# Optimization experiments

Measured on AMD Instinct MI355X. Metric: run time of the kernel, lower is better.

Reference implementation:

```python
import jax, jax.numpy as jnp
import numpy as np

B, C, H = 64, 64, 32

def _pm_cross_pairs(ks):
    # Replicates PM_cross(2, ks): pairs (i, i+j) ordered by gap j=1..ks-1, then i.
    a, b = [], []
    for j in range(1, ks):
        for i in range(ks - j):
            a.append(i)
            b.append(i + j)
    return np.array(a, dtype=np.int32), np.array(b, dtype=np.int32)

def setup_inputs() -> dict:
    key = jax.random.key(0)
    k1, k2 = jax.random.split(key)
    ia, ib = _pm_cross_pairs(H)           # 496 pairs for H=32
    hk = ia.shape[0] + 2 * H              # 560
    x = jax.random.normal(k1, (B, C, H, H), dtype=jnp.float32)
    weight = 0.1 * jax.random.normal(k2, (C, H, hk, H), dtype=jnp.float32)
    return {"x": x, "weight": weight, "idx_a": jnp.asarray(ia), "idx_b": jnp.asarray(ib)}

def reference(x, weight, idx_a, idx_b):
    # cross-term products along last axis: [B,C,H,P]
    cross = x[..., idx_a] * x[..., idx_b]
    feat = jnp.concatenate([x, x * x, cross], axis=-1)  # [B,C,H,Hk]
    # per-(channel,row) grouped matmul
    return jnp.einsum('bcij,cijo->bcio', feat, weight)
```

## Files before the change

kernel.cpp:

```cpp
#include <hip/hip_runtime.h>

#define NB 64
#define NC 64
#define NH 32
#define HK 560
#define NOCT 96
#define NCHUNK 12
#define XSTR 57

typedef __bf16 bf16x8 __attribute__((ext_vector_type(8)));
typedef float f32x4 __attribute__((ext_vector_type(4)));

__global__ __launch_bounds__(256, 5) void hconv_kernel(
    const float* __restrict__ x, const float* __restrict__ w,
    const int* __restrict__ idx_a, const int* __restrict__ idx_b,
    float* __restrict__ out)
{
    __shared__ float s_x[NB * XSTR];
    __shared__ unsigned s_desc[NOCT];
    __shared__ __align__(16) unsigned short s_wT[2][32][72];

    const int t = threadIdx.x;
    const int g = blockIdx.x;
    const int c = g >> 5, i = g & 31;

    {
        const int xrow = t >> 2, seg = t & 3;
        const float* xr = x + (((size_t)xrow * NC + c) * NH + i) * NH + seg * 8;
        float4 v0 = *(const float4*)(xr);
        float4 v1 = *(const float4*)(xr + 4);
        float* dst = &s_x[xrow * XSTR + 8 + seg * 8];
        dst[0] = v0.x; dst[1] = v0.y; dst[2] = v0.z; dst[3] = v0.w;
        dst[4] = v1.x; dst[5] = v1.y; dst[6] = v1.z; dst[7] = v1.w;
        if (seg == 0) {
            float* r0 = &s_x[xrow * XSTR];
            #pragma unroll
            for (int m = 0; m < 8; ++m) {
                r0[m] = 0.0f;
                r0[40 + m] = 0.0f;
                r0[48 + m] = 1.0f;
            }
        }
    }

    if (t < NOCT) {
        unsigned pa, pb, ko;
        if (t < 4)      { pa = 8u + 8u * t; pb = 48u; ko = 8u * t; }
        else if (t < 8) { unsigned u = t - 4; pa = pb = 8u + 8u * u; ko = 32u + 8u * u; }
        else if (t < 84) {
            unsigned q = t - 8, j, a;
            if (q < 28)      { j = 1 + q / 4;         a = q % 4; }
            else if (q < 52) { j = 8 + (q - 28) / 3;  a = (q - 28) % 3; }
            else if (q < 68) { j = 16 + (q - 52) / 2; a = (q - 52) % 2; }
            else             { j = 24 + (q - 68);     a = 0; }
            ko = 64u + (j - 1) * 32u - (j * (j - 1)) / 2u + 8u * a;
            pa = 8u + 8u * a; pb = pa + j;
            if (ko > 552u) { unsigned s = ko - 552u; ko = 552u; pa -= s; pb -= s; }
        } else { pa = 0u; pb = 0u; ko = 0u; }
        s_desc[t] = pa | (pb << 6) | (ko << 12);
    }

    const int wv = t >> 6, lane = t & 63;
    const int lr = lane & 15, lq = lane >> 4;
    const int arow = wv * 16 + lr;
    const int wo = t & 31;
    const int wkg = t >> 5;
    const float* wbase = w + (size_t)(c * NH + i) * HK * NH;
    const float* xrp = &s_x[arow * XSTR];

    __syncthreads();

    unsigned sd[NCHUNK];
    #pragma unroll
    for (int ch = 0; ch < NCHUNK; ++ch) sd[ch] = s_desc[ch * 8 + wkg] >> 12;

    float p0[8], p1[8];

    auto wload = [&](int ch, float* pv) {
        const float* p = wbase + (size_t)sd[ch] * NH + wo;
        #pragma unroll
        for (int r = 0; r < 8; ++r) pv[r] = p[r * NH];
    };
    auto wstore = [&](int bufi, const float* pv) {
        bf16x8 v;
        #pragma unroll
        for (int r = 0; r < 8; ++r) v[r] = (__bf16)pv[r];
        *(bf16x8*)&s_wT[bufi][wo][wkg * 8] = v;
    };

    f32x4 acc0 = {0.f, 0.f, 0.f, 0.f};
    f32x4 acc1 = {0.f, 0.f, 0.f, 0.f};

    auto mfma_chunk = [&](int ch, int bufi) {
        #pragma unroll
        for (int ks = 0; ks < 2; ++ks) {
            const unsigned d = s_desc[ch * 8 + ks * 4 + lq];
            const float* pA = xrp + (d & 63u);
            const float* pB = xrp + ((d >> 6) & 63u);
            bf16x8 a;
            #pragma unroll
            for (int j = 0; j < 8; ++j)
                a[j] = (__bf16)(pA[j] * pB[j]);
            bf16x8 b0 = *(const bf16x8*)&s_wT[bufi][lr][ks * 32 + lq * 8];
            bf16x8 b1 = *(const bf16x8*)&s_wT[bufi][16 + lr][ks * 32 + lq * 8];
            acc0 = __builtin_amdgcn_mfma_f32_16x16x32_bf16(a, b0, acc0, 0, 0, 0);
            acc1 = __builtin_amdgcn_mfma_f32_16x16x32_bf16(a, b1, acc1, 0, 0, 0);
        }
    };

    wload(0, p0);
    wload(1, p1);
    wstore(0, p0);
    __syncthreads();

    for (int it = 0; it < 6; ++it) {
        const int ca = 2 * it, cb = 2 * it + 1;
        wload(ca + 2 < NCHUNK ? ca + 2 : NCHUNK - 1, p0);
        mfma_chunk(ca, 0);
        wstore(1, p1);
        __syncthreads();
        wload(cb + 2 < NCHUNK ? cb + 2 : NCHUNK - 1, p1);
        mfma_chunk(cb, 1);
        wstore(0, p0);
        __syncthreads();
    }

    #pragma unroll
    for (int r = 0; r < 4; ++r) {
        const int b = wv * 16 + lq * 4 + r;
        float* op = out + (((size_t)b * NC + c) * NH + i) * NH;
        op[lr] = acc0[r];
        op[16 + lr] = acc1[r];
    }
}

extern "C" void kernel_launch(void* const* d_in, const int* in_sizes, int n_in,
                              void* d_out, int out_size, void* d_ws, size_t ws_size,
                              hipStream_t stream) {
    const float* x = (const float*)d_in[0];
    const float* w = (const float*)d_in[1];
    const int* idx_a = (const int*)d_in[2];
    const int* idx_b = (const int*)d_in[3];
    float* out = (float*)d_out;
    hconv_kernel<<<dim3(NC * NH), dim3(256), 0, stream>>>(x, w, idx_a, idx_b, out);
}
```

Baseline: 234.5 us.

## Split K across waves with register-direct weight loads and LDS reduction

Each wave now owns a slice of the K chunks and computes all 64 batch rows for all 32 outputs. Weights go from global memory straight into registers as MFMA B fragments, so the shared-memory transposed weight buffer and the per-chunk barriers are gone. A final LDS reduction across the four waves produces the output, which is written with float4 stores. The cost is more accumulator registers (launch bounds lowered to 4) and each wave computing the A-side products for every row, plus an extra reduction pass.

```diff
diff --git a/kernel.cpp b/kernel.cpp
--- a/kernel.cpp
+++ b/kernel.cpp
@@ -5,20 +5,19 @@
 #define NH 32
 #define HK 560
 #define NOCT 96
-#define NCHUNK 12
 #define XSTR 57
 
 typedef __bf16 bf16x8 __attribute__((ext_vector_type(8)));
 typedef float f32x4 __attribute__((ext_vector_type(4)));
 
-__global__ __launch_bounds__(256, 5) void hconv_kernel(
+__global__ __launch_bounds__(256, 4) void hconv_kernel(
     const float* __restrict__ x, const float* __restrict__ w,
     const int* __restrict__ idx_a, const int* __restrict__ idx_b,
     float* __restrict__ out)
 {
-    __shared__ float s_x[NB * XSTR];
-    __shared__ unsigned s_desc[NOCT];
-    __shared__ __align__(16) unsigned short s_wT[2][32][72];
+    __shared__ __align__(16) float smem[4 * 64 * 33];
+    float* s_x = smem;
+    unsigned* s_desc = (unsigned*)&smem[NB * XSTR];
 
     const int t = threadIdx.x;
     const int g = blockIdx.x;
@@ -45,92 +44,110 @@
 
     if (t < NOCT) {
         unsigned pa, pb, ko;
-        if (t < 4)      { pa = 8u + 8u * t; pb = 48u; ko = 8u * t; }
-        else if (t < 8) { unsigned u = t - 4; pa = pb = 8u + 8u * u; ko = 32u + 8u * u; }
-        else if (t < 84) {
-            unsigned q = t - 8, j, a;
-            if (q < 28)      { j = 1 + q / 4;         a = q % 4; }
-            else if (q < 52) { j = 8 + (q - 28) / 3;  a = (q - 28) % 3; }
-            else if (q < 68) { j = 16 + (q - 52) / 2; a = (q - 52) % 2; }
-            else             { j = 24 + (q - 68);     a = 0; }
+        const int mm = t % 24, ws = t / 24;
+        const int q = mm * 4 + ws;
+        if (mm >= 21)   { pa = 0u; pb = 0u; ko = 0u; }
+        else if (q < 4) { pa = 8u + 8u * q; pb = 48u; ko = 8u * q; }
+        else if (q < 8) { unsigned u = q - 4; pa = pb = 8u + 8u * u; ko = 32u + 8u * u; }
+        else {
+            unsigned qq = q - 8, j, a;
+            if (qq < 28)      { j = 1 + qq / 4;         a = qq % 4; }
+            else if (qq < 52) { j = 8 + (qq - 28) / 3;  a = (qq - 28) % 3; }
+            else if (qq < 68) { j = 16 + (qq - 52) / 2; a = (qq - 52) % 2; }
+            else              { j = 24 + (qq - 68);     a = 0; }
             ko = 64u + (j - 1) * 32u - (j * (j - 1)) / 2u + 8u * a;
             pa = 8u + 8u * a; pb = pa + j;
-            if (ko > 552u) { unsigned s = ko - 552u; ko = 552u; pa -= s; pb -= s; }
-        } else { pa = 0u; pb = 0u; ko = 0u; }
+            if (ko > 552u) { unsigned sh = ko - 552u; ko = 552u; pa -= sh; pb -= sh; }
+        }
         s_desc[t] = pa | (pb << 6) | (ko << 12);
     }
 
     const int wv = t >> 6, lane = t & 63;
     const int lr = lane & 15, lq = lane >> 4;
-    const int arow = wv * 16 + lr;
-    const int wo = t & 31;
-    const int wkg = t >> 5;
     const float* wbase = w + (size_t)(c * NH + i) * HK * NH;
-    const float* xrp = &s_x[arow * XSTR];
 
     __syncthreads();
 
-    unsigned sd[NCHUNK];
+    unsigned d6[6];
     #pragma unroll
-    for (int ch = 0; ch < NCHUNK; ++ch) sd[ch] = s_desc[ch * 8 + wkg] >> 12;
+    for (int k = 0; k < 6; ++k)
+        d6[k] = s_desc[(3 * wv + (k >> 1)) * 8 + (k & 1) * 4 + lq];
 
-    float p0[8], p1[8];
+    f32x4 acc[4][2];
+    #pragma unroll
+    for (int r = 0; r < 4; ++r) {
+        acc[r][0] = (f32x4){0.f, 0.f, 0.f, 0.f};
+        acc[r][1] = (f32x4){0.f, 0.f, 0.f, 0.f};
+    }
 
-    auto wload = [&](int ch, float* pv) {
-        const float* p = wbase + (size_t)sd[ch] * NH + wo;
-        #pragma unroll
-        for (int r = 0; r < 8; ++r) pv[r] = p[r * NH];
-    };
-    auto wstore = [&](int bufi, const float* pv) {
-        bf16x8 v;
-        #pragma unroll
-        for (int r = 0; r < 8; ++r) v[r] = (__bf16)pv[r];
-        *(bf16x8*)&s_wT[bufi][wo][wkg * 8] = v;
-    };
+    float fA[16], fB[16];
 
-    f32x4 acc0 = {0.f, 0.f, 0.f, 0.f};
-    f32x4 acc1 = {0.f, 0.f, 0.f, 0.f};
+#define LOADH(FBUF, K) { \
+    const float* wp_ = wbase + (size_t)(d6[K] >> 12) * NH + lr; \
+    _Pragma("unroll") \
+    for (int r_ = 0; r_ < 8; ++r_) { \
+        FBUF[r_]     = wp_[r_ * NH]; \
+        FBUF[8 + r_] = wp_[r_ * NH + 16]; } }
 
-    auto mfma_chunk = [&](int ch, int bufi) {
-        #pragma unroll
-        for (int ks = 0; ks < 2; ++ks) {
-            const unsigned d = s_desc[ch * 8 + ks * 4 + lq];
-            const float* pA = xrp + (d & 63u);
-            const float* pB = xrp + ((d >> 6) & 63u);
-            bf16x8 a;
-            #pragma unroll
-            for (int j = 0; j < 8; ++j)
-                a[j] = (__bf16)(pA[j] * pB[j]);
-            bf16x8 b0 = *(const bf16x8*)&s_wT[bufi][lr][ks * 32 + lq * 8];
-            bf16x8 b1 = *(const bf16x8*)&s_wT[bufi][16 + lr][ks * 32 + lq * 8];
-            acc0 = __builtin_amdgcn_mfma_f32_16x16x32_bf16(a, b0, acc0, 0, 0, 0);
-            acc1 = __builtin_amdgcn_mfma_f32_16x16x32_bf16(a, b1, acc1, 0, 0, 0);
-        }
-    };
+#define STEP(FBUF, K, KN, DOLOAD) { \
+    bf16x8 b0_, b1_; \
+    _Pragma("unroll") \
+    for (int j_ = 0; j_ < 8; ++j_) { \
+        b0_[j_] = (__bf16)FBUF[j_]; \
+        b1_[j_] = (__bf16)FBUF[8 + j_]; } \
+    if (DOLOAD) LOADH(FBUF, KN); \
+    const unsigned d_ = d6[K]; \
+    _Pragma("unroll") \
+    for (int rt_ = 0; rt_ < 4; ++rt_) { \
+        const float* xr_ = &s_x[(rt_ * 16 + lr) * XSTR]; \
+        const float* qa_ = xr_ + (d_ & 63u); \
+        const float* qb_ = xr_ + ((d_ >> 6) & 63u); \
+        bf16x8 a_; \
+        _Pragma("unroll") \
+        for (int j_ = 0; j_ < 8; ++j_) a_[j_] = (__bf16)(qa_[j_] * qb_[j_]); \
+        acc[rt_][0] = __builtin_amdgcn_mfma_f32_16x16x32_bf16(a_, b0_, acc[rt_][0], 0, 0, 0); \
+        acc[rt_][1] = __builtin_amdgcn_mfma_f32_16x16x32_bf16(a_, b1_, acc[rt_][1], 0, 0, 0); } }
 
-    wload(0, p0);
-    wload(1, p1);
-    wstore(0, p0);
+    LOADH(fA, 0);
+    LOADH(fB, 1);
+    STEP(fA, 0, 2, 1);
+    STEP(fB, 1, 3, 1);
+    STEP(fA, 2, 4, 1);
+    STEP(fB, 3, 5, 1);
+    STEP(fA, 4, 0, 0);
+    STEP(fB, 5, 0, 0);
+
+#undef STEP
+#undef LOADH
+
     __syncthreads();
 
-    for (int it = 0; it < 6; ++it) {
-        const int ca = 2 * it, cb = 2 * it + 1;
-        wload(ca + 2 < NCHUNK ? ca + 2 : NCHUNK - 1, p0);
-        mfma_chunk(ca, 0);
-        wstore(1, p1);
-        __syncthreads();
-        wload(cb + 2 < NCHUNK ? cb + 2 : NCHUNK - 1, p1);
-        mfma_chunk(cb, 1);
-        wstore(0, p0);
-        __syncthreads();
-    }
+    #pragma unroll
+    for (int rt = 0; rt < 4; ++rt)
+        #pragma unroll
+        for (int nh = 0; nh < 2; ++nh)
+            #pragma unroll
+            for (int r = 0; r < 4; ++r)
+                smem[(wv * NB + rt * 16 + lq * 4 + r) * 33 + nh * 16 + lr] =
+                    acc[rt][nh][r];
 
-    #pragma unroll
-    for (int r = 0; r < 4; ++r) {
-        const int b = wv * 16 + lq * 4 + r;
-        float* op = out + (((size_t)b * NC + c) * NH + i) * NH;
-        op[lr] = acc0[r];
-        op[16 + lr] = acc1[r];
+    __syncthreads();
+
+    {
+        const int b = t >> 2, m0 = (t & 3) * 8;
+        float s0[8];
+        #pragma unroll
+        for (int m = 0; m < 8; ++m) s0[m] = smem[b * 33 + m0 + m];
+        #pragma unroll
+        for (int wv2 = 1; wv2 < 4; ++wv2)
+            #pragma unroll
+            for (int m = 0; m < 8; ++m)
+                s0[m] += smem[(wv2 * NB + b) * 33 + m0 + m];
+        float* op = out + (((size_t)b * NC + c) * NH + i) * NH + m0;
+        float4 o0 = {s0[0], s0[1], s0[2], s0[3]};
+        float4 o1 = {s0[4], s0[5], s0[6], s0[7]};
+        *(float4*)op = o0;
+        *(float4*)(op + 4) = o1;
     }
 }
 
```

Result: faster. 228.4 us (-2.6%).
